# Kernel optimization log

Measured on AMD Instinct MI355X. Metric: run time of the kernel, lower is better.

## Reference

```python
import jax, jax.numpy as jnp
import numpy as np

N_NODES = 100000
N_EDGES = 1200000
N_FEAT = 128
HID = 64
PROJ = 32
BN_EPS = 1e-5


def setup_inputs() -> dict:
    key = jax.random.key(0)
    ks = jax.random.split(key, 20)
    s = 0.02
    inp = {
        'x': jax.random.normal(ks[0], (N_NODES, N_FEAT), dtype=jnp.float32),
        'edge_index': jax.random.randint(ks[1], (2, N_EDGES), 0, N_NODES, dtype=jnp.int64),
        # feat_mlp: Linear(n_feat, hid) + BatchNorm1d(hid) (eval mode)
        'W1': jax.random.normal(ks[2], (N_FEAT, HID), jnp.float32) * s,
        'b1': jnp.zeros((HID,), jnp.float32),
        'gamma': jnp.ones((HID,), jnp.float32),
        'beta': jnp.zeros((HID,), jnp.float32),
        'rmean': jnp.zeros((HID,), jnp.float32),
        'rvar': jnp.ones((HID,), jnp.float32),
        # GCN layers: lin weights + bias
        'gW0': jax.random.normal(ks[3], (N_FEAT, HID), jnp.float32) * s,
        'gb0': jnp.zeros((HID,), jnp.float32),
        'gW1': jax.random.normal(ks[4], (HID, HID), jnp.float32) * s,
        'gb1': jnp.zeros((HID,), jnp.float32),
        'gW2': jax.random.normal(ks[5], (HID, HID), jnp.float32) * s,
        'gb2': jnp.zeros((HID,), jnp.float32),
        # gate: Linear(2*hid, 1) + sigmoid
        'gateW': jax.random.normal(ks[6], (2 * HID, 1), jnp.float32) * s,
        'gateb': jnp.zeros((1,), jnp.float32),
        # projection: Linear(hid,hid) -> relu -> Linear(hid,proj)
        'pW1': jax.random.normal(ks[7], (HID, HID), jnp.float32) * s,
        'pb1': jnp.zeros((HID,), jnp.float32),
        'pW2': jax.random.normal(ks[8], (HID, PROJ), jnp.float32) * s,
        'pb2': jnp.zeros((PROJ,), jnp.float32),
        # classifier: Linear(hid, 1)
        'cW': jax.random.normal(ks[9], (HID, 1), jnp.float32) * s,
        'cb': jnp.zeros((1,), jnp.float32),
    }
    return inp


def reference(x, edge_index, W1, b1, gamma, beta, rmean, rvar,
              gW0, gb0, gW1, gb1, gW2, gb2,
              gateW, gateb, pW1, pb1, pW2, pb2, cW, cb):
    N = x.shape[0]
    # --- GCN normalization (add self loops, symmetric deg^-1/2 norm) ---
    loop = jnp.arange(N, dtype=edge_index.dtype)
    src = jnp.concatenate([edge_index[0], loop])  # [E+N]
    dst = jnp.concatenate([edge_index[1], loop])
    deg = jax.ops.segment_sum(jnp.ones(src.shape[0], x.dtype), dst, num_segments=N)
    dinv = jax.lax.rsqrt(deg)  # deg >= 1 due to self loops
    norm = dinv[src] * dinv[dst]  # [E+N]

    def gcn(h, W, b):
        hw = h @ W                       # [N, out]
        msg = hw[src] * norm[:, None]    # gather + scale, [E+N, out]
        agg = jax.ops.segment_sum(msg, dst, num_segments=N)
        return agg + b

    # --- MLP branch (BatchNorm in eval mode, dropout = identity) ---
    h = x @ W1 + b1
    h = (h - rmean) * jax.lax.rsqrt(rvar + BN_EPS) * gamma + beta
    h_mlp = jax.nn.relu(h)

    # --- graph branch: stacked GCN layers with relu ---
    hg = x
    for W, b in ((gW0, gb0), (gW1, gb1), (gW2, gb2)):
        hg = jax.nn.relu(gcn(hg, W, b))

    # --- sigmoid gating fusion ---
    gate = jax.nn.sigmoid(jnp.concatenate([h_mlp, hg], axis=1) @ gateW + gateb)  # [N,1]
    h_fused = gate * hg + (1.0 - gate) * h_mlp

    # --- projection head + classifier ---
    z_proj = jax.nn.relu(h_fused @ pW1 + pb1) @ pW2 + pb2
    logits = (h_fused @ cW + cb).reshape(-1)
    return logits, z_proj
```

## Files before the change

kernel.cpp:

```cpp
#include <hip/hip_runtime.h>
#include <hip/hip_bf16.h>


#define HID 64

typedef unsigned short ushort_t;
typedef unsigned int uint_t;
typedef short bf16x8 __attribute__((ext_vector_type(8)));
typedef float f32x4 __attribute__((ext_vector_type(4)));

__device__ __forceinline__ float bflo(uint_t u) {
    union { unsigned u; float f; } c;
    c.u = u << 16;
    return c.f;
}
__device__ __forceinline__ float bfhi(uint_t u) {
    union { unsigned u; float f; } c;
    c.u = u & 0xFFFF0000u;
    return c.f;
}
__device__ __forceinline__ float bf2f(ushort_t u) {
    union { unsigned u; float f; } c;
    c.u = ((unsigned)u) << 16;
    return c.f;
}
__device__ __forceinline__ ushort_t f2bf(float f) {
    union { float f; unsigned u; } c;
    c.f = f;
    unsigned u = c.u;
    unsigned r = (u + 0x7FFFu + ((u >> 16) & 1u)) >> 16;
    return (ushort_t)r;
}

__global__ __launch_bounds__(256) void deg_kernel(const int* __restrict__ dst, int E,
                                                  int* __restrict__ deg) {
    int e = blockIdx.x * 256 + threadIdx.x;
    if (e < E) atomicAdd(&deg[dst[e]], 1);
}

__global__ __launch_bounds__(256) void scanA(const int* __restrict__ deg,
                                             int* __restrict__ excl,
                                             int* __restrict__ partials, int N) {
    __shared__ int s[256];
    int t = threadIdx.x;
    int i = blockIdx.x * 256 + t;
    int v = (i < N) ? deg[i] : 0;
    s[t] = v;
    __syncthreads();
    for (int off = 1; off < 256; off <<= 1) {
        int u = (t >= off) ? s[t - off] : 0;
        __syncthreads();
        s[t] += u;
        __syncthreads();
    }
    if (i < N) excl[i] = s[t] - v;
    if (t == 255) partials[blockIdx.x] = s[255];
}

__global__ __launch_bounds__(512) void scanB(int* __restrict__ partials, int P) {
    __shared__ int s[512];
    int t = threadIdx.x;
    int v = (t < P) ? partials[t] : 0;
    s[t] = v;
    __syncthreads();
    for (int off = 1; off < 512; off <<= 1) {
        int u = (t >= off) ? s[t - off] : 0;
        __syncthreads();
        s[t] += u;
        __syncthreads();
    }
    if (t < P) partials[t] = s[t] - v;
}

__global__ __launch_bounds__(256) void scanC(const int* __restrict__ excl,
                                             const int* __restrict__ partials,
                                             const int* __restrict__ deg,
                                             int* __restrict__ row_start,
                                             int* __restrict__ cursor,
                                             float* __restrict__ dinv, int N, int E) {
    int i = blockIdx.x * 256 + threadIdx.x;
    if (i < N) {
        int rs = excl[i] + partials[blockIdx.x];
        row_start[i] = rs;
        cursor[i] = rs;
        dinv[i] = rsqrtf((float)deg[i] + 1.0f);
        if (i == 0) row_start[N] = E;
    }
}

__global__ __launch_bounds__(256) void fill_csr2(const int* __restrict__ src,
                                                 const int* __restrict__ dst, int E,
                                                 int* __restrict__ cursor,
                                                 int* __restrict__ csr_src, int N) {
    int rng = blockIdx.x & 7;
    int gr  = blockIdx.x >> 3;
    int lo = (int)(((long long)N * rng) >> 3);
    int hi = (int)(((long long)N * (rng + 1)) >> 3);
    int nthr = (gridDim.x >> 3) * 256;
    for (int e = gr * 256 + threadIdx.x; e < E; e += nthr) {
        int d = dst[e];
        if (d >= lo && d < hi) {
            int pos = atomicAdd(&cursor[d], 1);
            csr_src[pos] = src[e];
        }
    }
}

__global__ __launch_bounds__(256) void prep_wfrag(const float* __restrict__ W1,
                                                  const float* __restrict__ gW0,
                                                  ushort_t* __restrict__ fW,
                                                  ushort_t* __restrict__ fG) {
    int i = blockIdx.x * 256 + threadIdx.x;
    if (i >= 16384) return;
    int w    = i >> 13;
    int j    = i & 8191;
    int e    = j & 7;
    int lane = (j >> 3) & 63;
    int nt   = (j >> 9) & 3;
    int kc   = (j >> 11) & 3;
    int k   = kc * 32 + (lane >> 4) * 8 + e;
    int col = nt * 16 + (lane & 15);
    const float* W = (w == 0) ? W1 : gW0;
    ushort_t v = f2bf(W[k * 64 + col]);
    if (w == 0) fW[j] = v; else fG[j] = v;
}

__global__ __launch_bounds__(256) void rowgemm_mfma(
    const float* __restrict__ x,
    const ushort_t* __restrict__ fW, const ushort_t* __restrict__ fG,
    const float* __restrict__ b1, const float* __restrict__ gamma,
    const float* __restrict__ beta, const float* __restrict__ rmean,
    const float* __restrict__ rvar, const float* __restrict__ dinv,
    ushort_t* __restrict__ h_mlp, ushort_t* __restrict__ hw_s, int N) {
    int tid = threadIdx.x, lane = tid & 63, wid = tid >> 6;
    int rb = (blockIdx.x * 4 + wid) * 16;
    if (rb >= N) return;
    int r0 = lane & 15, kg = lane >> 4;
    int arow = rb + r0;
    if (arow > N - 1) arow = N - 1;
    const float* xbase = x + (size_t)arow * 128 + kg * 8;

    f32x4 accA[4] = {{0,0,0,0},{0,0,0,0},{0,0,0,0},{0,0,0,0}};
    f32x4 accB[4] = {{0,0,0,0},{0,0,0,0},{0,0,0,0},{0,0,0,0}};

#pragma unroll
    for (int kc = 0; kc < 4; ++kc) {
        float4 xa = *(const float4*)(xbase + kc * 32);
        float4 xb = *(const float4*)(xbase + kc * 32 + 4);
        bf16x8 a;
        a[0] = (short)f2bf(xa.x); a[1] = (short)f2bf(xa.y);
        a[2] = (short)f2bf(xa.z); a[3] = (short)f2bf(xa.w);
        a[4] = (short)f2bf(xb.x); a[5] = (short)f2bf(xb.y);
        a[6] = (short)f2bf(xb.z); a[7] = (short)f2bf(xb.w);
#pragma unroll
        for (int nt = 0; nt < 4; ++nt) {
            bf16x8 bw = *(const bf16x8*)(fW + ((size_t)(kc * 4 + nt) * 64 + lane) * 8);
            bf16x8 bg = *(const bf16x8*)(fG + ((size_t)(kc * 4 + nt) * 64 + lane) * 8);
            accA[nt] = __builtin_amdgcn_mfma_f32_16x16x32_bf16(a, bw, accA[nt], 0, 0, 0);
            accB[nt] = __builtin_amdgcn_mfma_f32_16x16x32_bf16(a, bg, accB[nt], 0, 0, 0);
        }
    }

    float dv[4];
    bool okr[4];
#pragma unroll
    for (int rr = 0; rr < 4; ++rr) {
        int row = rb + kg * 4 + rr;
        okr[rr] = (row < N);
        dv[rr] = okr[rr] ? dinv[row] : 0.f;
    }
#pragma unroll
    for (int nt = 0; nt < 4; ++nt) {
        int col = nt * 16 + r0;
        float esc = gamma[col] * rsqrtf(rvar[col] + 1e-5f);
        float ebi = beta[col] + (b1[col] - rmean[col]) * esc;
#pragma unroll
        for (int rr = 0; rr < 4; ++rr) {
            int row = rb + kg * 4 + rr;
            if (okr[rr]) {
                float h = fmaxf(fmaf(accA[nt][rr], esc, ebi), 0.f);
                h_mlp[(size_t)row * HID + col] = f2bf(h);
                hw_s[(size_t)row * HID + col] = f2bf(accB[nt][rr] * dv[rr]);
            }
        }
    }
}

__device__ __forceinline__ void stageWT(float* sWT, const float* W, int tid) {
    for (int i = tid; i < 4096; i += 256) {
        int k = i >> 6, c = i & 63;
        sWT[c * 64 + ((((k >> 2) ^ (c & 7)) << 2) | (k & 3))] = W[i];
    }
}

template <int MODE>
__global__ __launch_bounds__(256) void agg2(
    const ushort_t* __restrict__ hw_s, const int* __restrict__ row_start,
    const int* __restrict__ csr_src, const float* __restrict__ dinv,
    const float* __restrict__ gb,
    const float* __restrict__ Wn,
    const ushort_t* __restrict__ h_mlp,
    const float* __restrict__ gateW, const float* __restrict__ gateb,
    const float* __restrict__ pW1, const float* __restrict__ pb1,
    const float* __restrict__ pW2, const float* __restrict__ pb2,
    const float* __restrict__ cW, const float* __restrict__ cb,
    ushort_t* __restrict__ out_bf,
    float* __restrict__ logits, float* __restrict__ zproj, int N) {
    extern __shared__ float smem[];
    float* sWT  = smem;
    float* sW2T = smem + 4096;
    float* sbuf = smem + (MODE == 0 ? 4096 : 4096 + 2048);
    int tid = threadIdx.x, lane = tid & 63, wid = tid >> 6;
    float* shg = sbuf + wid * 256;

    if (MODE == 0) {
        stageWT(sWT, Wn, tid);
    } else {
        stageWT(sWT, pW1, tid);
        for (int i = tid; i < 2048; i += 256) {
            int k = i >> 5, c = i & 31;
            sW2T[c * 64 + ((((k >> 2) ^ (c & 7)) << 2) | (k & 3))] = pW2[i];
        }
    }
    __syncthreads();

    int g = lane >> 4, sub = lane & 15;
    float4 gb4 = ((const float4*)gb)[sub];
    float gWa = 0.f, gWb = 0.f, pb1v = 0.f, pb2v = 0.f, cWv = 0.f, gb0v = 0.f, cb0v = 0.f;
    if (MODE == 1) {
        gWa = gateW[lane];
        gWb = gateW[64 + lane];
        pb1v = pb1[lane];
        pb2v = pb2[lane & 31];
        cWv = cW[lane];
        gb0v = gateb[0];
        cb0v = cb[0];
    }

    int npacks = (N + 3) >> 2;
    for (int pack = blockIdx.x * 4 + wid; pack < npacks; pack += gridDim.x * 4) {
        int d0 = pack * 4;
        int d = d0 + g;
        bool ok = d < N;
        int dd = ok ? d : N - 1;
        int rs = row_start[dd];
        int deg = ok ? (row_start[dd + 1] - rs) : 0;

        uint2 sv = ((const uint2*)(hw_s + (size_t)dd * HID))[sub];
        float ax, ay, az, aw;
        if (ok) { ax = bflo(sv.x); ay = bfhi(sv.x); az = bflo(sv.y); aw = bfhi(sv.y); }
        else    { ax = ay = az = aw = 0.f; }

        int dmax = deg;
        dmax = max(dmax, __shfl_xor(dmax, 16, 64));
        dmax = max(dmax, __shfl_xor(dmax, 32, 64));

        for (int base = 0; base < dmax; base += 16) {
            int idx = (base + sub < deg) ? csr_src[rs + base + sub] : 0;
            int m = dmax - base;
            if (m > 16) m = 16;
            for (int j = 0; j < m; j += 4) {
                int s0 = __shfl(idx, (g << 4) | (j + 0), 64);
                int s1 = __shfl(idx, (g << 4) | (j + 1), 64);
                int s2 = __shfl(idx, (g << 4) | (j + 2), 64);
                int s3 = __shfl(idx, (g << 4) | (j + 3), 64);
                bool v0 = base + j + 0 < deg, v1 = base + j + 1 < deg;
                bool v2 = base + j + 2 < deg, v3 = base + j + 3 < deg;
                uint2 g0 = ((const uint2*)(hw_s + (size_t)s0 * HID))[sub];
                uint2 g1 = ((const uint2*)(hw_s + (size_t)s1 * HID))[sub];
                uint2 g2 = ((const uint2*)(hw_s + (size_t)s2 * HID))[sub];
                uint2 g3 = ((const uint2*)(hw_s + (size_t)s3 * HID))[sub];
                if (v0) { ax += bflo(g0.x); ay += bfhi(g0.x); az += bflo(g0.y); aw += bfhi(g0.y); }
                if (v1) { ax += bflo(g1.x); ay += bfhi(g1.x); az += bflo(g1.y); aw += bfhi(g1.y); }
                if (v2) { ax += bflo(g2.x); ay += bfhi(g2.x); az += bflo(g2.y); aw += bfhi(g2.y); }
                if (v3) { ax += bflo(g3.x); ay += bfhi(g3.x); az += bflo(g3.y); aw += bfhi(g3.y); }
            }
        }

        float dv = dinv[dd];
        float h0 = fmaxf(fmaf(ax, dv, gb4.x), 0.f);
        float h1 = fmaxf(fmaf(ay, dv, gb4.y), 0.f);
        float h2 = fmaxf(fmaf(az, dv, gb4.z), 0.f);
        float h3 = fmaxf(fmaf(aw, dv, gb4.w), 0.f);
        if (!ok) { h0 = h1 = h2 = h3 = 0.f; }
        *(float4*)&shg[g * 64 + 4 * sub] = make_float4(h0, h1, h2, h3);

        if (MODE == 0) {
            float a0 = 0.f, a1 = 0.f, a2 = 0.f, a3 = 0.f;
#pragma unroll 4
            for (int kq = 0; kq < 16; ++kq) {
                float4 w4 = *(const float4*)&sWT[lane * 64 + ((kq ^ (lane & 7)) << 2)];
                float4 x0 = *(const float4*)&shg[0 * 64 + kq * 4];
                float4 x1 = *(const float4*)&shg[1 * 64 + kq * 4];
                float4 x2 = *(const float4*)&shg[2 * 64 + kq * 4];
                float4 x3 = *(const float4*)&shg[3 * 64 + kq * 4];
                a0 = fmaf(x0.x, w4.x, a0); a0 = fmaf(x0.y, w4.y, a0);
                a0 = fmaf(x0.z, w4.z, a0); a0 = fmaf(x0.w, w4.w, a0);
                a1 = fmaf(x1.x, w4.x, a1); a1 = fmaf(x1.y, w4.y, a1);
                a1 = fmaf(x1.z, w4.z, a1); a1 = fmaf(x1.w, w4.w, a1);
                a2 = fmaf(x2.x, w4.x, a2); a2 = fmaf(x2.y, w4.y, a2);
                a2 = fmaf(x2.z, w4.z, a2); a2 = fmaf(x2.w, w4.w, a2);
                a3 = fmaf(x3.x, w4.x, a3); a3 = fmaf(x3.y, w4.y, a3);
                a3 = fmaf(x3.z, w4.z, a3); a3 = fmaf(x3.w, w4.w, a3);
            }
            float dv0 = __shfl(dv, 0, 64);
            float dv1 = __shfl(dv, 16, 64);
            float dv2 = __shfl(dv, 32, 64);
            float dv3 = __shfl(dv, 48, 64);
            if (d0 + 0 < N) out_bf[(size_t)(d0 + 0) * HID + lane] = f2bf(a0 * dv0);
            if (d0 + 1 < N) out_bf[(size_t)(d0 + 1) * HID + lane] = f2bf(a1 * dv1);
            if (d0 + 2 < N) out_bf[(size_t)(d0 + 2) * HID + lane] = f2bf(a2 * dv2);
            if (d0 + 3 < N) out_bf[(size_t)(d0 + 3) * HID + lane] = f2bf(a3 * dv3);
        } else {
            float hm0 = (d0 + 0 < N) ? bf2f(h_mlp[(size_t)(d0 + 0) * HID + lane]) : 0.f;
            float hm1 = (d0 + 1 < N) ? bf2f(h_mlp[(size_t)(d0 + 1) * HID + lane]) : 0.f;
            float hm2 = (d0 + 2 < N) ? bf2f(h_mlp[(size_t)(d0 + 2) * HID + lane]) : 0.f;
            float hm3 = (d0 + 3 < N) ? bf2f(h_mlp[(size_t)(d0 + 3) * HID + lane]) : 0.f;
            float hg0 = shg[0 * 64 + lane];
            float hg1 = shg[1 * 64 + lane];
            float hg2 = shg[2 * 64 + lane];
            float hg3 = shg[3 * 64 + lane];
            float p0 = fmaf(hm0, gWa, hg0 * gWb);
            float p1 = fmaf(hm1, gWa, hg1 * gWb);
            float p2 = fmaf(hm2, gWa, hg2 * gWb);
            float p3 = fmaf(hm3, gWa, hg3 * gWb);
#pragma unroll
            for (int mm = 32; mm >= 1; mm >>= 1) {
                p0 += __shfl_xor(p0, mm, 64);
                p1 += __shfl_xor(p1, mm, 64);
                p2 += __shfl_xor(p2, mm, 64);
                p3 += __shfl_xor(p3, mm, 64);
            }
            float gate0 = 1.f / (1.f + expf(-(p0 + gb0v)));
            float gate1 = 1.f / (1.f + expf(-(p1 + gb0v)));
            float gate2 = 1.f / (1.f + expf(-(p2 + gb0v)));
            float gate3 = 1.f / (1.f + expf(-(p3 + gb0v)));
            float hf0 = gate0 * hg0 + (1.f - gate0) * hm0;
            float hf1 = gate1 * hg1 + (1.f - gate1) * hm1;
            float hf2 = gate2 * hg2 + (1.f - gate2) * hm2;
            float hf3 = gate3 * hg3 + (1.f - gate3) * hm3;
            shg[0 * 64 + lane] = hf0;
            shg[1 * 64 + lane] = hf1;
            shg[2 * 64 + lane] = hf2;
            shg[3 * 64 + lane] = hf3;
            float t0 = 0.f, t1 = 0.f, t2 = 0.f, t3 = 0.f;
#pragma unroll 4
            for (int kq = 0; kq < 16; ++kq) {
                float4 w4 = *(const float4*)&sWT[lane * 64 + ((kq ^ (lane & 7)) << 2)];
                float4 x0 = *(const float4*)&shg[0 * 64 + kq * 4];
                float4 x1 = *(const float4*)&shg[1 * 64 + kq * 4];
                float4 x2 = *(const float4*)&shg[2 * 64 + kq * 4];
                float4 x3 = *(const float4*)&shg[3 * 64 + kq * 4];
                t0 = fmaf(x0.x, w4.x, t0); t0 = fmaf(x0.y, w4.y, t0);
                t0 = fmaf(x0.z, w4.z, t0); t0 = fmaf(x0.w, w4.w, t0);
                t1 = fmaf(x1.x, w4.x, t1); t1 = fmaf(x1.y, w4.y, t1);
                t1 = fmaf(x1.z, w4.z, t1); t1 = fmaf(x1.w, w4.w, t1);
                t2 = fmaf(x2.x, w4.x, t2); t2 = fmaf(x2.y, w4.y, t2);
                t2 = fmaf(x2.z, w4.z, t2); t2 = fmaf(x2.w, w4.w, t2);
                t3 = fmaf(x3.x, w4.x, t3); t3 = fmaf(x3.y, w4.y, t3);
                t3 = fmaf(x3.z, w4.z, t3); t3 = fmaf(x3.w, w4.w, t3);
            }
            t0 = fmaxf(t0 + pb1v, 0.f);
            t1 = fmaxf(t1 + pb1v, 0.f);
            t2 = fmaxf(t2 + pb1v, 0.f);
            t3 = fmaxf(t3 + pb1v, 0.f);
            shg[0 * 64 + lane] = t0;
            shg[1 * 64 + lane] = t1;
            shg[2 * 64 + lane] = t2;
            shg[3 * 64 + lane] = t3;
            int c2 = lane & 31, hh = lane >> 5;
            float z0 = 0.f, z1 = 0.f, z2 = 0.f, z3 = 0.f;
#pragma unroll 4
            for (int kq8 = 0; kq8 < 8; ++kq8) {
                int kq = hh * 8 + kq8;
                float4 w4 = *(const float4*)&sW2T[c2 * 64 + ((kq ^ (c2 & 7)) << 2)];
                float4 x0 = *(const float4*)&shg[0 * 64 + kq * 4];
                float4 x1 = *(const float4*)&shg[1 * 64 + kq * 4];
                float4 x2 = *(const float4*)&shg[2 * 64 + kq * 4];
                float4 x3 = *(const float4*)&shg[3 * 64 + kq * 4];
                z0 = fmaf(x0.x, w4.x, z0); z0 = fmaf(x0.y, w4.y, z0);
                z0 = fmaf(x0.z, w4.z, z0); z0 = fmaf(x0.w, w4.w, z0);
                z1 = fmaf(x1.x, w4.x, z1); z1 = fmaf(x1.y, w4.y, z1);
                z1 = fmaf(x1.z, w4.z, z1); z1 = fmaf(x1.w, w4.w, z1);
                z2 = fmaf(x2.x, w4.x, z2); z2 = fmaf(x2.y, w4.y, z2);
                z2 = fmaf(x2.z, w4.z, z2); z2 = fmaf(x2.w, w4.w, z2);
                z3 = fmaf(x3.x, w4.x, z3); z3 = fmaf(x3.y, w4.y, z3);
                z3 = fmaf(x3.z, w4.z, z3); z3 = fmaf(x3.w, w4.w, z3);
            }
            z0 += __shfl_xor(z0, 32, 64);
            z1 += __shfl_xor(z1, 32, 64);
            z2 += __shfl_xor(z2, 32, 64);
            z3 += __shfl_xor(z3, 32, 64);
            if (lane < 32) {
                if (d0 + 0 < N) zproj[(size_t)(d0 + 0) * 32 + c2] = z0 + pb2v;
                if (d0 + 1 < N) zproj[(size_t)(d0 + 1) * 32 + c2] = z1 + pb2v;
                if (d0 + 2 < N) zproj[(size_t)(d0 + 2) * 32 + c2] = z2 + pb2v;
                if (d0 + 3 < N) zproj[(size_t)(d0 + 3) * 32 + c2] = z3 + pb2v;
            }
            float q0 = hf0 * cWv, q1 = hf1 * cWv, q2 = hf2 * cWv, q3 = hf3 * cWv;
#pragma unroll
            for (int mm = 32; mm >= 1; mm >>= 1) {
                q0 += __shfl_xor(q0, mm, 64);
                q1 += __shfl_xor(q1, mm, 64);
                q2 += __shfl_xor(q2, mm, 64);
                q3 += __shfl_xor(q3, mm, 64);
            }
            if (lane == 0) {
                if (d0 + 0 < N) logits[d0 + 0] = q0 + cb0v;
                if (d0 + 1 < N) logits[d0 + 1] = q1 + cb0v;
                if (d0 + 2 < N) logits[d0 + 2] = q2 + cb0v;
                if (d0 + 3 < N) logits[d0 + 3] = q3 + cb0v;
            }
        }
    }
}

extern "C" void kernel_launch(void* const* d_in, const int* in_sizes, int n_in,
                              void* d_out, int out_size, void* d_ws, size_t ws_size,
                              hipStream_t stream) {
    const float* x     = (const float*)d_in[0];
    const int*   edge  = (const int*)d_in[1];
    const float* W1    = (const float*)d_in[2];
    const float* b1    = (const float*)d_in[3];
    const float* gamma = (const float*)d_in[4];
    const float* beta  = (const float*)d_in[5];
    const float* rmean = (const float*)d_in[6];
    const float* rvar  = (const float*)d_in[7];
    const float* gW0   = (const float*)d_in[8];
    const float* gb0   = (const float*)d_in[9];
    const float* gW1   = (const float*)d_in[10];
    const float* gb1   = (const float*)d_in[11];
    const float* gW2   = (const float*)d_in[12];
    const float* gb2   = (const float*)d_in[13];
    const float* gateW = (const float*)d_in[14];
    const float* gateb = (const float*)d_in[15];
    const float* pW1   = (const float*)d_in[16];
    const float* pb1   = (const float*)d_in[17];
    const float* pW2   = (const float*)d_in[18];
    const float* pb2   = (const float*)d_in[19];
    const float* cW    = (const float*)d_in[20];
    const float* cb    = (const float*)d_in[21];

    const int N = in_sizes[0] / 128;
    const int E = in_sizes[1] / 2;
    const int* e_src = edge;
    const int* e_dst = edge + E;

    char* ws = (char*)d_ws;
    size_t o = 0;
    auto alloc = [&](size_t bytes) {
        void* p = ws + o;
        o += (bytes + 15) & ~(size_t)15;
        return p;
    };
    int* deg       = (int*)alloc((size_t)N * 4);
    int* excl      = (int*)alloc((size_t)N * 4);
    int* partials  = (int*)alloc(512 * 4);
    int* row_start = (int*)alloc(((size_t)N + 1) * 4);
    int* cursor    = (int*)alloc((size_t)N * 4);
    int* csr_src   = (int*)alloc((size_t)E * 4);
    float* dinv    = (float*)alloc((size_t)N * 4);
    ushort_t* fW   = (ushort_t*)alloc(8192 * 2);
    ushort_t* fG   = (ushort_t*)alloc(8192 * 2);
    ushort_t* h_mlp= (ushort_t*)alloc((size_t)N * 64 * 2);
    ushort_t* hwA  = (ushort_t*)alloc((size_t)N * 64 * 2);
    ushort_t* hwB  = (ushort_t*)alloc((size_t)N * 64 * 2);

    float* logits = (float*)d_out;
    float* zproj  = (float*)d_out + N;

    const int nblkN = (N + 255) / 256;
    const int nblkE = (E + 255) / 256;
    const int nblkG = (N + 63) / 64;
    const int blk0  = 2048;
    const int blk1  = 1280;
    const size_t lds0 = (4096 + 4 * 256) * 4;
    const size_t lds1 = (4096 + 2048 + 4 * 256) * 4;

    hipMemsetAsync(deg, 0, (size_t)N * sizeof(int), stream);
    deg_kernel<<<nblkE, 256, 0, stream>>>(e_dst, E, deg);
    scanA<<<nblkN, 256, 0, stream>>>(deg, excl, partials, N);
    scanB<<<1, 512, 0, stream>>>(partials, nblkN);
    scanC<<<nblkN, 256, 0, stream>>>(excl, partials, deg, row_start, cursor, dinv, N, E);
    fill_csr2<<<2048, 256, 0, stream>>>(e_src, e_dst, E, cursor, csr_src, N);

    prep_wfrag<<<64, 256, 0, stream>>>(W1, gW0, fW, fG);
    rowgemm_mfma<<<nblkG, 256, 0, stream>>>(x, fW, fG, b1, gamma, beta, rmean,
                                            rvar, dinv, h_mlp, hwA, N);

    agg2<0><<<blk0, 256, lds0, stream>>>(hwA, row_start, csr_src, dinv, gb0,
                                         gW1, nullptr, nullptr, nullptr,
                                         nullptr, nullptr, nullptr, nullptr,
                                         nullptr, nullptr, hwB, nullptr, nullptr, N);
    agg2<0><<<blk0, 256, lds0, stream>>>(hwB, row_start, csr_src, dinv, gb1,
                                         gW2, nullptr, nullptr, nullptr,
                                         nullptr, nullptr, nullptr, nullptr,
                                         nullptr, nullptr, hwA, nullptr, nullptr, N);
    agg2<1><<<blk1, 256, lds1, stream>>>(hwA, row_start, csr_src, dinv, gb2,
                                         nullptr, h_mlp, gateW, gateb,
                                         pW1, pb1, pW2, pb2, cW, cb,
                                         nullptr, logits, zproj, N);
}
```

Baseline: 313.3 us.

## Process GCN aggregation nodes in degree-sorted order to cut wave divergence

Adds a counting sort of nodes by in-degree (histogram, scan, scatter into a permutation array). The three aggregation kernels now walk nodes through this permutation, so the four nodes sharing a wave have similar degrees. The goal is to cut idle lanes in the neighbour-gather loop, which runs to the wave's maximum degree. In exchange it adds three small kernels and a memset, an extra indirection per node, and scattered rather than sequential output writes and h_mlp reads.

Result: slower. 331.6 us (+5.8%).

```diff
diff --git a/kernel.cpp b/kernel.cpp
--- a/kernel.cpp
+++ b/kernel.cpp
@@ -104,6 +104,50 @@
             csr_src[pos] = src[e];
         }
     }
+}
+
+__global__ __launch_bounds__(256) void sortA(const int* __restrict__ deg,
+                                             int* __restrict__ bins, int N) {
+    __shared__ int h[64];
+    int t = threadIdx.x;
+    if (t < 64) h[t] = 0;
+    __syncthreads();
+    int i = blockIdx.x * 256 + t;
+    if (i < N) atomicAdd(&h[min(deg[i], 63)], 1);
+    __syncthreads();
+    if (t < 64 && h[t] > 0) atomicAdd(&bins[t], h[t]);
+}
+
+__global__ void sortB(int* __restrict__ bins) {
+    int t = threadIdx.x;
+    int orig = bins[t];
+    int v = orig;
+    for (int off = 1; off < 64; off <<= 1) {
+        int u = __shfl_up(v, off, 64);
+        if (t >= off) v += u;
+    }
+    bins[t] = v - orig;
+}
+
+__global__ __launch_bounds__(256) void sortC(const int* __restrict__ deg,
+                                             int* __restrict__ cursor64,
+                                             int* __restrict__ perm, int N) {
+    __shared__ int h[64];
+    __shared__ int gbase[64];
+    int t = threadIdx.x;
+    if (t < 64) h[t] = 0;
+    __syncthreads();
+    int i = blockIdx.x * 256 + t;
+    int d = 0, r = 0;
+    bool ok = i < N;
+    if (ok) {
+        d = min(deg[i], 63);
+        r = atomicAdd(&h[d], 1);
+    }
+    __syncthreads();
+    if (t < 64) gbase[t] = (h[t] > 0) ? atomicAdd(&cursor64[t], h[t]) : 0;
+    __syncthreads();
+    if (ok) perm[gbase[d] + r] = i;
 }
 
 __global__ __launch_bounds__(256) void prep_wfrag(const float* __restrict__ W1,
@@ -197,6 +241,7 @@
 __global__ __launch_bounds__(256) void agg2(
     const ushort_t* __restrict__ hw_s, const int* __restrict__ row_start,
     const int* __restrict__ csr_src, const float* __restrict__ dinv,
+    const int* __restrict__ perm,
     const float* __restrict__ gb,
     const float* __restrict__ Wn,
     const ushort_t* __restrict__ h_mlp,
@@ -240,9 +285,9 @@
     int npacks = (N + 3) >> 2;
     for (int pack = blockIdx.x * 4 + wid; pack < npacks; pack += gridDim.x * 4) {
         int d0 = pack * 4;
-        int d = d0 + g;
-        bool ok = d < N;
-        int dd = ok ? d : N - 1;
+        int li = d0 + g;
+        bool ok = li < N;
+        int dd = perm[ok ? li : N - 1];
         int rs = row_start[dd];
         int deg = ok ? (row_start[dd + 1] - rs) : 0;
 
@@ -285,6 +330,11 @@
         if (!ok) { h0 = h1 = h2 = h3 = 0.f; }
         *(float4*)&shg[g * 64 + 4 * sub] = make_float4(h0, h1, h2, h3);
 
+        int dd0 = __shfl(dd, 0, 64);
+        int dd1 = __shfl(dd, 16, 64);
+        int dd2 = __shfl(dd, 32, 64);
+        int dd3 = __shfl(dd, 48, 64);
+
         if (MODE == 0) {
             float a0 = 0.f, a1 = 0.f, a2 = 0.f, a3 = 0.f;
 #pragma unroll 4
@@ -307,15 +357,15 @@
             float dv1 = __shfl(dv, 16, 64);
             float dv2 = __shfl(dv, 32, 64);
             float dv3 = __shfl(dv, 48, 64);
-            if (d0 + 0 < N) out_bf[(size_t)(d0 + 0) * HID + lane] = f2bf(a0 * dv0);
-            if (d0 + 1 < N) out_bf[(size_t)(d0 + 1) * HID + lane] = f2bf(a1 * dv1);
-            if (d0 + 2 < N) out_bf[(size_t)(d0 + 2) * HID + lane] = f2bf(a2 * dv2);
-            if (d0 + 3 < N) out_bf[(size_t)(d0 + 3) * HID + lane] = f2bf(a3 * dv3);
+            if (d0 + 0 < N) out_bf[(size_t)dd0 * HID + lane] = f2bf(a0 * dv0);
+            if (d0 + 1 < N) out_bf[(size_t)dd1 * HID + lane] = f2bf(a1 * dv1);
+            if (d0 + 2 < N) out_bf[(size_t)dd2 * HID + lane] = f2bf(a2 * dv2);
+            if (d0 + 3 < N) out_bf[(size_t)dd3 * HID + lane] = f2bf(a3 * dv3);
         } else {
-            float hm0 = (d0 + 0 < N) ? bf2f(h_mlp[(size_t)(d0 + 0) * HID + lane]) : 0.f;
-            float hm1 = (d0 + 1 < N) ? bf2f(h_mlp[(size_t)(d0 + 1) * HID + lane]) : 0.f;
-            float hm2 = (d0 + 2 < N) ? bf2f(h_mlp[(size_t)(d0 + 2) * HID + lane]) : 0.f;
-            float hm3 = (d0 + 3 < N) ? bf2f(h_mlp[(size_t)(d0 + 3) * HID + lane]) : 0.f;
+            float hm0 = (d0 + 0 < N) ? bf2f(h_mlp[(size_t)dd0 * HID + lane]) : 0.f;
+            float hm1 = (d0 + 1 < N) ? bf2f(h_mlp[(size_t)dd1 * HID + lane]) : 0.f;
+            float hm2 = (d0 + 2 < N) ? bf2f(h_mlp[(size_t)dd2 * HID + lane]) : 0.f;
+            float hm3 = (d0 + 3 < N) ? bf2f(h_mlp[(size_t)dd3 * HID + lane]) : 0.f;
             float hg0 = shg[0 * 64 + lane];
             float hg1 = shg[1 * 64 + lane];
             float hg2 = shg[2 * 64 + lane];
@@ -392,10 +442,10 @@
             z2 += __shfl_xor(z2, 32, 64);
             z3 += __shfl_xor(z3, 32, 64);
             if (lane < 32) {
-                if (d0 + 0 < N) zproj[(size_t)(d0 + 0) * 32 + c2] = z0 + pb2v;
-                if (d0 + 1 < N) zproj[(size_t)(d0 + 1) * 32 + c2] = z1 + pb2v;
-                if (d0 + 2 < N) zproj[(size_t)(d0 + 2) * 32 + c2] = z2 + pb2v;
-                if (d0 + 3 < N) zproj[(size_t)(d0 + 3) * 32 + c2] = z3 + pb2v;
+                if (d0 + 0 < N) zproj[(size_t)dd0 * 32 + c2] = z0 + pb2v;
+                if (d0 + 1 < N) zproj[(size_t)dd1 * 32 + c2] = z1 + pb2v;
+                if (d0 + 2 < N) zproj[(size_t)dd2 * 32 + c2] = z2 + pb2v;
+                if (d0 + 3 < N) zproj[(size_t)dd3 * 32 + c2] = z3 + pb2v;
             }
             float q0 = hf0 * cWv, q1 = hf1 * cWv, q2 = hf2 * cWv, q3 = hf3 * cWv;
 #pragma unroll
@@ -406,10 +456,10 @@
                 q3 += __shfl_xor(q3, mm, 64);
             }
             if (lane == 0) {
-                if (d0 + 0 < N) logits[d0 + 0] = q0 + cb0v;
-                if (d0 + 1 < N) logits[d0 + 1] = q1 + cb0v;
-                if (d0 + 2 < N) logits[d0 + 2] = q2 + cb0v;
-                if (d0 + 3 < N) logits[d0 + 3] = q3 + cb0v;
+                if (d0 + 0 < N) logits[dd0] = q0 + cb0v;
+                if (d0 + 1 < N) logits[dd1] = q1 + cb0v;
+                if (d0 + 2 < N) logits[dd2] = q2 + cb0v;
+                if (d0 + 3 < N) logits[dd3] = q3 + cb0v;
             }
         }
     }
@@ -460,6 +510,8 @@
     int* cursor    = (int*)alloc((size_t)N * 4);
     int* csr_src   = (int*)alloc((size_t)E * 4);
     float* dinv    = (float*)alloc((size_t)N * 4);
+    int* bins      = (int*)alloc(64 * 4);
+    int* perm      = (int*)alloc((size_t)N * 4);
     ushort_t* fW   = (ushort_t*)alloc(8192 * 2);
     ushort_t* fG   = (ushort_t*)alloc(8192 * 2);
     ushort_t* h_mlp= (ushort_t*)alloc((size_t)N * 64 * 2);
@@ -478,25 +530,30 @@
     const size_t lds1 = (4096 + 2048 + 4 * 256) * 4;
 
     hipMemsetAsync(deg, 0, (size_t)N * sizeof(int), stream);
+    hipMemsetAsync(bins, 0, 64 * sizeof(int), stream);
     deg_kernel<<<nblkE, 256, 0, stream>>>(e_dst, E, deg);
     scanA<<<nblkN, 256, 0, stream>>>(deg, excl, partials, N);
     scanB<<<1, 512, 0, stream>>>(partials, nblkN);
     scanC<<<nblkN, 256, 0, stream>>>(excl, partials, deg, row_start, cursor, dinv, N, E);
     fill_csr2<<<2048, 256, 0, stream>>>(e_src, e_dst, E, cursor, csr_src, N);
 
+    sortA<<<nblkN, 256, 0, stream>>>(deg, bins, N);
+    sortB<<<1, 64, 0, stream>>>(bins);
+    sortC<<<nblkN, 256, 0, stream>>>(deg, bins, perm, N);
+
     prep_wfrag<<<64, 256, 0, stream>>>(W1, gW0, fW, fG);
     rowgemm_mfma<<<nblkG, 256, 0, stream>>>(x, fW, fG, b1, gamma, beta, rmean,
                                             rvar, dinv, h_mlp, hwA, N);
 
-    agg2<0><<<blk0, 256, lds0, stream>>>(hwA, row_start, csr_src, dinv, gb0,
+    agg2<0><<<blk0, 256, lds0, stream>>>(hwA, row_start, csr_src, dinv, perm, gb0,
                                          gW1, nullptr, nullptr, nullptr,
                                          nullptr, nullptr, nullptr, nullptr,
                                          nullptr, nullptr, hwB, nullptr, nullptr, N);
-    agg2<0><<<blk0, 256, lds0, stream>>>(hwB, row_start, csr_src, dinv, gb1,
+    agg2<0><<<blk0, 256, lds0, stream>>>(hwB, row_start, csr_src, dinv, perm, gb1,
                                          gW2, nullptr, nullptr, nullptr,
                                          nullptr, nullptr, nullptr, nullptr,
                                          nullptr, nullptr, hwA, nullptr, nullptr, N);
-    agg2<1><<<blk1, 256, lds1, stream>>>(hwA, row_start, csr_src, dinv, gb2,
+    agg2<1><<<blk1, 256, lds1, stream>>>(hwA, row_start, csr_src, dinv, perm, gb2,
                                          nullptr, h_mlp, gateW, gateb,
                                          pW1, pb1, pW2, pb2, cW, cb,
                                          nullptr, logits, zproj, N);
```
